# Kernel tuning notes

Measured on AMD Instinct MI355X. Metric: run time of the kernel, lower is better.

Reference implementation:

```python
import jax, jax.numpy as jnp
import numpy as np


def binarize(t):
    # torch.where(t > 0, +1, -1)
    return jnp.where(t > 0, jnp.float32(1.0), jnp.float32(-1.0))


def setup_inputs() -> dict:
    key = jax.random.key(0)
    k1, k2, k3 = jax.random.split(key, 3)
    N, D_IN, D_OUT = 8192, 4096, 4096
    x = jax.random.normal(k1, (N, D_IN), dtype=jnp.float32)
    weight = jax.random.normal(k2, (D_OUT, D_IN), dtype=jnp.float32) * 0.02
    bias = jax.random.normal(k3, (D_OUT,), dtype=jnp.float32) * 0.02
    return {"x": x, "weight": weight, "bias": bias}


def reference(x, weight, bias):
    # Binarize input and weight to +/-1, then standard float linear: y = bx @ bw^T + b
    bx = binarize(x)          # [N, D_in]
    bw = binarize(weight)     # [D_out, D_in]
    return jnp.einsum('ni,oi->no', bx, bw) + bias
```

## Files before the change

kernel.cpp:

```cpp
#include <hip/hip_runtime.h>
#include <stdint.h>

using i32x4 = __attribute__((ext_vector_type(4))) int;
using i32x8 = __attribute__((ext_vector_type(8))) int;
using f32x4 = __attribute__((ext_vector_type(4))) float;

#define M_ROWS 8192
#define N_COLS 4096
#define K_DIM  4096
#define KB_ROW 2048
#define BM 256
#define BN 256
#define TKB 128
#define NT (KB_ROW / TKB)
#define SC1 0x7F7F7F7F

#define XDW   ((size_t)M_ROWS * K_DIM / 8)
#define TOTDW (((size_t)(M_ROWS + N_COLS)) * K_DIM / 8)

__device__ __forceinline__ unsigned pack8(float4 a, float4 b) {
  unsigned neg =
      ((a.x > 0.f ? 0u : 1u) << 3)  | ((a.y > 0.f ? 0u : 1u) << 7)  |
      ((a.z > 0.f ? 0u : 1u) << 11) | ((a.w > 0.f ? 0u : 1u) << 15) |
      ((b.x > 0.f ? 0u : 1u) << 19) | ((b.y > 0.f ? 0u : 1u) << 23) |
      ((b.z > 0.f ? 0u : 1u) << 27) | ((b.w > 0.f ? 0u : 1u) << 31);
  return 0x22222222u | neg;
}

__global__ __launch_bounds__(256) void binarize_fp4_fused(
    const float4* __restrict__ x, const float4* __restrict__ w,
    unsigned* __restrict__ out) {
  size_t u = (size_t)blockIdx.x * blockDim.x + threadIdx.x;
  size_t stride = (size_t)gridDim.x * blockDim.x;
  for (; u < TOTDW / 2; u += stride) {
    size_t d = u * 2;
    const float4* s;
    size_t j;
    if (d < XDW) { s = x; j = d * 2; }
    else         { s = w; j = (d - XDW) * 2; }
    float4 f0 = s[j], f1 = s[j + 1], f2 = s[j + 2], f3 = s[j + 3];
    out[d]     = pack8(f0, f1);
    out[d + 1] = pack8(f2, f3);
  }
}

#define GLOAD(gsrc, ldst)                                                    \
  __builtin_amdgcn_global_load_lds(                                          \
      (const __attribute__((address_space(1))) void*)(gsrc),                 \
      (__attribute__((address_space(3))) void*)(ldst), 16, 0, 0)


#define STG_A(NB, KBo, KH)                                                   \
  GLOAD(aS0 + (KBo) + (KH) * 64, As + (NB) + (KH) * 16384 + dstW);           \
  GLOAD(aS1 + (KBo) + (KH) * 64, As + (NB) + (KH) * 16384 + 8192 + dstW)

#define STG_B(NB, KBo, KH)                                                   \
  GLOAD(bS0 + (KBo) + (KH) * 64, Bs + (NB) + (KH) * 16384 + dstW);           \
  GLOAD(bS1 + (KBo) + (KH) * 64, Bs + (NB) + (KH) * 16384 + 8192 + dstW)

#define VM4BAR                                                               \
  asm volatile("s_waitcnt vmcnt(4)" ::: "memory");                           \
  __builtin_amdgcn_s_barrier();

#define VM0BAR                                                               \
  asm volatile("s_waitcnt vmcnt(0)" ::: "memory");                           \
  __builtin_amdgcn_s_barrier();

#define DO_PHASE(BUFOFF, KHOFF, STAGE_STMT, CLOSE_STMT)                      \
  {                                                                          \
    STAGE_STMT                                                               \
    _Pragma("unroll")                                                        \
    for (int nf = 0; nf < 4; ++nf)                                           \
      *(i32x4*)&bf8[nf] =                                                    \
          *(const i32x4*)(Bs + (BUFOFF) + (KHOFF) + bRdOff + nf * 1024);     \
    __builtin_amdgcn_s_setprio(1);                                           \
    _Pragma("unroll")                                                        \
    for (int fr = 0; fr < 8; ++fr) {                                         \
      *(i32x4*)&af8[fr & 1] =                                                \
          *(const i32x4*)(As + (BUFOFF) + (KHOFF) + aRdOff + fr * 1024);     \
      _Pragma("unroll")                                                      \
      for (int nf = 0; nf < 4; ++nf)                                         \
        acc[fr][nf] = __builtin_amdgcn_mfma_scale_f32_16x16x128_f8f6f4(      \
            af8[fr & 1], bf8[nf], acc[fr][nf], 4, 4, 0, SC1, 0, SC1);        \
    }                                                                        \
    __builtin_amdgcn_s_setprio(0);                                           \
    CLOSE_STMT                                                               \
  }

#define TILE(BUF, NBUF, KBo)                                                 \
  DO_PHASE(BUF, 0,     STG_A(NBUF, KBo, 0); STG_B(NBUF, KBo, 0);, VM4BAR)    \
  DO_PHASE(BUF, 16384, STG_A(NBUF, KBo, 1); STG_B(NBUF, KBo, 1);, VM4BAR)

#define TILE_LAST(BUF)                                                       \
  DO_PHASE(BUF, 0, , VM0BAR)                                                 \
  DO_PHASE(BUF, 16384, , )

__global__ __launch_bounds__(512, 2) void bgemm_fp4_2bar(
    const unsigned char* __restrict__ xa, const unsigned char* __restrict__ wb,
    const float* __restrict__ bias, float* __restrict__ y) {
  __shared__ __align__(16) unsigned char As[65536];
  __shared__ __align__(16) unsigned char Bs[65536];

  const int tid  = threadIdx.x;
  const int lane = tid & 63;
  const int w8   = tid >> 6;
  const int wr   = w8 >> 2;
  const int wc   = w8 & 3;

  const int id = blockIdx.x;
  const int sw = ((id & 7) << 6) | (id >> 3);
  const int by = sw >> 4;
  const int bx = sw & 15;
  const int m0 = by * BM;
  const int n0 = bx * BN;

  const int r0  = tid >> 2;
  const int gsl = (((tid & 3) ^ ((tid >> 3) & 3)) << 4);
  const unsigned char* aS0 = xa + (size_t)(m0 + r0) * KB_ROW + gsl;
  const unsigned char* aS1 = xa + (size_t)(m0 + 128 + r0) * KB_ROW + gsl;
  const unsigned char* bS0 = wb + (size_t)(n0 + r0) * KB_ROW + gsl;
  const unsigned char* bS1 = wb + (size_t)(n0 + 128 + r0) * KB_ROW + gsl;
  const int dstW = w8 * 1024;

  const int lr  = lane & 15;
  const int kq  = lane >> 4;
  const int rsw = (kq ^ ((lr >> 1) & 3)) << 4;
  const int aRdOff = (wr * 128 + lr) * 64 + rsw;
  const int bRdOff = (wc * 64 + lr) * 64 + rsw;

  f32x4 acc[8][4];
#pragma unroll
  for (int i = 0; i < 8; ++i)
#pragma unroll
    for (int j = 0; j < 4; ++j) acc[i][j] = (f32x4){0.f, 0.f, 0.f, 0.f};

  i32x8 af8[2], bf8[4];
#pragma unroll
  for (int i = 0; i < 2; ++i) af8[i] = (i32x8){0, 0, 0, 0, 0, 0, 0, 0};
#pragma unroll
  for (int i = 0; i < 4; ++i) bf8[i] = (i32x8){0, 0, 0, 0, 0, 0, 0, 0};

  STG_A(0, 0, 0);
  STG_B(0, 0, 0);
  STG_A(0, 0, 1);
  STG_B(0, 0, 1);
  asm volatile("s_waitcnt vmcnt(4)" ::: "memory");
  __builtin_amdgcn_s_barrier();

#pragma unroll 1
  for (int tp = 0; tp < 7; ++tp) {
    const int kb1 = tp * 256 + 128;
    const int kb2 = tp * 256 + 256;
    TILE(0, 32768, kb1)
    TILE(32768, 0, kb2)
  }
  TILE(0, 32768, 1920)
  TILE_LAST(32768)

  float bv[4];
#pragma unroll
  for (int nf = 0; nf < 4; ++nf) bv[nf] = bias[n0 + wc * 64 + nf * 16 + lr];
#pragma unroll
  for (int fr = 0; fr < 8; ++fr) {
#pragma unroll
    for (int j = 0; j < 4; ++j) {
      const int gr = m0 + wr * 128 + fr * 16 + kq * 4 + j;
      float* orow = y + (size_t)gr * N_COLS + n0 + wc * 64 + lr;
#pragma unroll
      for (int nf = 0; nf < 4; ++nf)
        orow[nf * 16] = acc[fr][nf][j] + bv[nf];
    }
  }
}

extern "C" void kernel_launch(void* const* d_in, const int* in_sizes, int n_in,
                              void* d_out, int out_size, void* d_ws, size_t ws_size,
                              hipStream_t stream) {
  const float* x    = (const float*)d_in[0];
  const float* wgt  = (const float*)d_in[1];
  const float* bias = (const float*)d_in[2];
  float* y = (float*)d_out;

  unsigned char* xa = (unsigned char*)d_ws;
  unsigned char* wb = xa + (size_t)M_ROWS * KB_ROW;

  binarize_fp4_fused<<<4096, 256, 0, stream>>>(
      (const float4*)x, (const float4*)wgt, (unsigned*)xa);

  bgemm_fp4_2bar<<<512, 512, 0, stream>>>(xa, wb, bias, y);
}
```

Before: 131.5 us.

## Switch FP4 GEMM to 32x32x64 scaled MFMA and widen binarize stores

The GEMM inner loop now uses the 32x32x64 scaled MFMA instead of 16x16x128. The per-wave tile is split into 4x2 fragments with new LDS read offsets and a matching epilogue layout. The larger MFMA is meant to cut LDS fragment reads per FLOP and the number of instructions issued. The binarize kernel now packs 32 values per thread and writes them with one 16-byte store, with a smaller grid, to lower store overhead. The risk is a wrong fragment or epilogue mapping, or bank conflicts, with the new read pattern.

Result: no change. 130.6 us (-0.7%).

```diff
diff --git a/kernel.cpp b/kernel.cpp
--- a/kernel.cpp
+++ b/kernel.cpp
@@ -1,9 +1,9 @@
 #include <hip/hip_runtime.h>
 #include <stdint.h>
 
-using i32x4 = __attribute__((ext_vector_type(4))) int;
-using i32x8 = __attribute__((ext_vector_type(8))) int;
-using f32x4 = __attribute__((ext_vector_type(4))) float;
+using i32x4  = __attribute__((ext_vector_type(4))) int;
+using i32x8  = __attribute__((ext_vector_type(8))) int;
+using f32x16 = __attribute__((ext_vector_type(16))) float;
 
 #define M_ROWS 8192
 #define N_COLS 4096
@@ -11,8 +11,6 @@
 #define KB_ROW 2048
 #define BM 256
 #define BN 256
-#define TKB 128
-#define NT (KB_ROW / TKB)
 #define SC1 0x7F7F7F7F
 
 #define XDW   ((size_t)M_ROWS * K_DIM / 8)
@@ -29,18 +27,23 @@
 
 __global__ __launch_bounds__(256) void binarize_fp4_fused(
     const float4* __restrict__ x, const float4* __restrict__ w,
-    unsigned* __restrict__ out) {
+    uint4* __restrict__ out) {
   size_t u = (size_t)blockIdx.x * blockDim.x + threadIdx.x;
   size_t stride = (size_t)gridDim.x * blockDim.x;
-  for (; u < TOTDW / 2; u += stride) {
-    size_t d = u * 2;
+  for (; u < TOTDW / 4; u += stride) {
+    size_t d = u * 4;
     const float4* s;
     size_t j;
     if (d < XDW) { s = x; j = d * 2; }
     else         { s = w; j = (d - XDW) * 2; }
     float4 f0 = s[j], f1 = s[j + 1], f2 = s[j + 2], f3 = s[j + 3];
-    out[d]     = pack8(f0, f1);
-    out[d + 1] = pack8(f2, f3);
+    float4 f4 = s[j + 4], f5 = s[j + 5], f6 = s[j + 6], f7 = s[j + 7];
+    uint4 o;
+    o.x = pack8(f0, f1);
+    o.y = pack8(f2, f3);
+    o.z = pack8(f4, f5);
+    o.w = pack8(f6, f7);
+    out[u] = o;
   }
 }
 
@@ -69,19 +72,22 @@
 #define DO_PHASE(BUFOFF, KHOFF, STAGE_STMT, CLOSE_STMT)                      \
   {                                                                          \
     STAGE_STMT                                                               \
-    _Pragma("unroll")                                                        \
-    for (int nf = 0; nf < 4; ++nf)                                           \
-      *(i32x4*)&bf8[nf] =                                                    \
-          *(const i32x4*)(Bs + (BUFOFF) + (KHOFF) + bRdOff + nf * 1024);     \
     __builtin_amdgcn_s_setprio(1);                                           \
     _Pragma("unroll")                                                        \
-    for (int fr = 0; fr < 8; ++fr) {                                         \
-      *(i32x4*)&af8[fr & 1] =                                                \
-          *(const i32x4*)(As + (BUFOFF) + (KHOFF) + aRdOff + fr * 1024);     \
+    for (int ks = 0; ks < 2; ++ks) {                                         \
       _Pragma("unroll")                                                      \
-      for (int nf = 0; nf < 4; ++nf)                                         \
-        acc[fr][nf] = __builtin_amdgcn_mfma_scale_f32_16x16x128_f8f6f4(      \
-            af8[fr & 1], bf8[nf], acc[fr][nf], 4, 4, 0, SC1, 0, SC1);        \
+      for (int nf = 0; nf < 2; ++nf)                                         \
+        *(i32x4*)&bf8[nf] = *(const i32x4*)(Bs + (BUFOFF) + (KHOFF) +        \
+                                            bBase + nf * 2048 + kv[ks]);     \
+      _Pragma("unroll")                                                      \
+      for (int mf = 0; mf < 4; ++mf) {                                       \
+        *(i32x4*)&af8[mf & 1] = *(const i32x4*)(As + (BUFOFF) + (KHOFF) +    \
+                                                aBase + mf * 2048 + kv[ks]); \
+        _Pragma("unroll")                                                    \
+        for (int nf = 0; nf < 2; ++nf)                                       \
+          acc[mf][nf] = __builtin_amdgcn_mfma_scale_f32_32x32x64_f8f6f4(     \
+              af8[mf & 1], bf8[nf], acc[mf][nf], 4, 4, 0, SC1, 0, SC1);      \
+      }                                                                      \
     }                                                                        \
     __builtin_amdgcn_s_setprio(0);                                           \
     CLOSE_STMT                                                               \
@@ -95,7 +101,7 @@
   DO_PHASE(BUF, 0, , VM0BAR)                                                 \
   DO_PHASE(BUF, 16384, , )
 
-__global__ __launch_bounds__(512, 2) void bgemm_fp4_2bar(
+__global__ __launch_bounds__(512, 2) void bgemm_fp4_32x32(
     const unsigned char* __restrict__ xa, const unsigned char* __restrict__ wb,
     const float* __restrict__ bias, float* __restrict__ y) {
   __shared__ __align__(16) unsigned char As[65536];
@@ -122,23 +128,29 @@
   const unsigned char* bS1 = wb + (size_t)(n0 + 128 + r0) * KB_ROW + gsl;
   const int dstW = w8 * 1024;
 
-  const int lr  = lane & 15;
-  const int kq  = lane >> 4;
-  const int rsw = (kq ^ ((lr >> 1) & 3)) << 4;
-  const int aRdOff = (wr * 128 + lr) * 64 + rsw;
-  const int bRdOff = (wc * 64 + lr) * 64 + rsw;
-
-  f32x4 acc[8][4];
-#pragma unroll
-  for (int i = 0; i < 8; ++i)
-#pragma unroll
-    for (int j = 0; j < 4; ++j) acc[i][j] = (f32x4){0.f, 0.f, 0.f, 0.f};
-
-  i32x8 af8[2], bf8[4];
-#pragma unroll
-  for (int i = 0; i < 2; ++i) af8[i] = (i32x8){0, 0, 0, 0, 0, 0, 0, 0};
-#pragma unroll
-  for (int i = 0; i < 4; ++i) bf8[i] = (i32x8){0, 0, 0, 0, 0, 0, 0, 0};
+  const int l31 = lane & 31;
+  const int lh  = lane >> 5;
+  const int rx  = (l31 >> 1) & 3;
+  int kv[2];
+  kv[0] = ((0 * 2 + lh) ^ rx) << 4;
+  kv[1] = ((1 * 2 + lh) ^ rx) << 4;
+  const int aBase = (wr * 128 + l31) * 64;
+  const int bBase = (wc * 64 + l31) * 64;
+
+  f32x16 acc[4][2];
+#pragma unroll
+  for (int i = 0; i < 4; ++i)
+#pragma unroll
+    for (int j = 0; j < 2; ++j)
+#pragma unroll
+      for (int e = 0; e < 16; ++e) acc[i][j][e] = 0.f;
+
+  i32x8 af8[2], bf8[2];
+#pragma unroll
+  for (int i = 0; i < 2; ++i) {
+    af8[i] = (i32x8){0, 0, 0, 0, 0, 0, 0, 0};
+    bf8[i] = (i32x8){0, 0, 0, 0, 0, 0, 0, 0};
+  }
 
   STG_A(0, 0, 0);
   STG_B(0, 0, 0);
@@ -157,18 +169,19 @@
   TILE(0, 32768, 1920)
   TILE_LAST(32768)
 
-  float bv[4];
-#pragma unroll
-  for (int nf = 0; nf < 4; ++nf) bv[nf] = bias[n0 + wc * 64 + nf * 16 + lr];
-#pragma unroll
-  for (int fr = 0; fr < 8; ++fr) {
-#pragma unroll
-    for (int j = 0; j < 4; ++j) {
-      const int gr = m0 + wr * 128 + fr * 16 + kq * 4 + j;
-      float* orow = y + (size_t)gr * N_COLS + n0 + wc * 64 + lr;
-#pragma unroll
-      for (int nf = 0; nf < 4; ++nf)
-        orow[nf * 16] = acc[fr][nf][j] + bv[nf];
+  float bv[2];
+#pragma unroll
+  for (int nf = 0; nf < 2; ++nf) bv[nf] = bias[n0 + wc * 64 + nf * 32 + l31];
+#pragma unroll
+  for (int mf = 0; mf < 4; ++mf) {
+#pragma unroll
+    for (int j = 0; j < 16; ++j) {
+      const int fr = (j & 3) + 8 * (j >> 2) + 4 * lh;
+      const int gr = m0 + wr * 128 + mf * 32 + fr;
+      float* orow = y + (size_t)gr * N_COLS + n0 + wc * 64 + l31;
+#pragma unroll
+      for (int nf = 0; nf < 2; ++nf)
+        orow[nf * 32] = acc[mf][nf][j] + bv[nf];
     }
   }
 }
@@ -184,8 +197,8 @@
   unsigned char* xa = (unsigned char*)d_ws;
   unsigned char* wb = xa + (size_t)M_ROWS * KB_ROW;
 
-  binarize_fp4_fused<<<4096, 256, 0, stream>>>(
-      (const float4*)x, (const float4*)wgt, (unsigned*)xa);
-
-  bgemm_fp4_2bar<<<512, 512, 0, stream>>>(xa, wb, bias, y);
-}
+  binarize_fp4_fused<<<3072, 256, 0, stream>>>(
+      (const float4*)x, (const float4*)wgt, (uint4*)xa);
+
+  bgemm_fp4_32x32<<<512, 512, 0, stream>>>(xa, wb, bias, y);
+}
```
